# Kernel optimization log

Measured on AMD Instinct MI355X. Metric: run time of the kernel, lower is better.

Reference implementation:

```python
import jax, jax.numpy as jnp
import numpy as np

N = 50000   # nodes
D = 128     # hidden_dim == in_dim
H = 4       # heads
C = 32      # hidden_dim // heads
L = 3       # message_layers
ET = 640000 # temporal edges
EH = 320000 # host edges


def layer_norm(x, g, b, eps=1e-5):
    m = x.mean(-1, keepdims=True)
    v = ((x - m) ** 2).mean(-1, keepdims=True)
    return (x - m) / jnp.sqrt(v + eps) * g + b


def transformer_conv(h, src, dst, e_emb, Wq, bq, Wk, bk, Wv, bv, We, Ws, bs):
    # PyG TransformerConv, concat=True, root_weight=True, beta=False
    n = h.shape[0]
    q = (h @ Wq + bq).reshape(n, H, C)
    k = (h @ Wk + bk).reshape(n, H, C)
    v = (h @ Wv + bv).reshape(n, H, C)
    ee = (e_emb @ We).reshape(-1, H, C)          # lin_edge has no bias
    kj = k[src] + ee                              # [E,H,C]
    a = (q[dst] * kj).sum(-1) / np.sqrt(C)        # [E,H]
    amax = jax.ops.segment_max(a, dst, num_segments=n)
    amax = jnp.where(jnp.isfinite(amax), amax, 0.0)
    ex = jnp.exp(a - amax[dst])
    den = jax.ops.segment_sum(ex, dst, num_segments=n)
    alpha = ex / (den[dst] + 1e-16)               # segment softmax over in-edges of dst
    msg = (v[src] + ee) * alpha[..., None]        # [E,H,C]
    out = jax.ops.segment_sum(msg, dst, num_segments=n).reshape(n, H * C)
    return out + h @ Ws + bs                      # root/skip connection


def mlp_head(h, W1, b1, g, bt, W2, b2):
    z = jax.nn.silu(h @ W1 + b1)
    z = layer_norm(z, g, bt)
    return z @ W2 + b2


def setup_inputs() -> dict:
    key = jax.random.key(0)
    ks = iter(jax.random.split(key, 80))
    nrm = lambda shape: jax.random.normal(next(ks), shape, jnp.float32) * 0.05
    inp = {}
    inp['x'] = jax.random.normal(next(ks), (N, D), jnp.float32)
    inp['edge_index_temporal'] = jax.random.randint(next(ks), (2, ET), 0, N)
    inp['edge_index_host'] = jax.random.randint(next(ks), (2, EH), 0, N)
    inp['edge_attr_temporal'] = jax.random.uniform(next(ks), (ET, 1), jnp.float32)
    inp['edge_attr_host'] = jax.random.normal(next(ks), (EH, 3), jnp.float32)
    # edge encoders
    inp['W_tedge'] = nrm((1, 4)); inp['b_tedge'] = jnp.zeros(4)
    inp['W_hedge'] = nrm((3, 4)); inp['b_hedge'] = jnp.zeros(4)
    # stacked conv params [L, ...] for temporal (_t) and host (_h) convs
    for s in ('t', 'h'):
        inp[f'Wq_{s}'] = nrm((L, D, D)); inp[f'bq_{s}'] = jnp.zeros((L, D))
        inp[f'Wk_{s}'] = nrm((L, D, D)); inp[f'bk_{s}'] = jnp.zeros((L, D))
        inp[f'Wv_{s}'] = nrm((L, D, D)); inp[f'bv_{s}'] = jnp.zeros((L, D))
        inp[f'We_{s}'] = nrm((L, 4, D))
        inp[f'Ws_{s}'] = nrm((L, D, D)); inp[f'bs_{s}'] = jnp.zeros((L, D))
    inp['norm_g'] = jnp.ones((L, D)); inp['norm_b'] = jnp.zeros((L, D))
    inp['fg'] = jnp.ones(D); inp['fb'] = jnp.zeros(D)
    inp['dW1'] = nrm((D, D)); inp['db1'] = jnp.zeros(D)
    inp['dg'] = jnp.ones(D); inp['dbt'] = jnp.zeros(D)
    inp['dW2'] = nrm((D, 3)); inp['db2'] = jnp.zeros(3)
    inp['sW1'] = nrm((D, D)); inp['sb1'] = jnp.zeros(D)
    inp['sg'] = jnp.ones(D); inp['sbt'] = jnp.zeros(D)
    inp['sW2'] = nrm((D, 3)); inp['sb2'] = jnp.zeros(3)
    return inp


def reference(x, edge_index_temporal, edge_index_host, edge_attr_temporal, edge_attr_host,
              W_tedge, b_tedge, W_hedge, b_hedge,
              Wq_t, bq_t, Wk_t, bk_t, Wv_t, bv_t, We_t, Ws_t, bs_t,
              Wq_h, bq_h, Wk_h, bk_h, Wv_h, bv_h, We_h, Ws_h, bs_h,
              norm_g, norm_b, fg, fb,
              dW1, db1, dg, dbt, dW2, db2,
              sW1, sb1, sg, sbt, sW2, sb2):
    te = edge_attr_temporal @ W_tedge + b_tedge   # [ET, edge_dim]
    he = edge_attr_host @ W_hedge + b_hedge       # [EH, edge_dim]
    st, dt_ = edge_index_temporal[0], edge_index_temporal[1]
    sh, dh = edge_index_host[0], edge_index_host[1]
    h = x
    for l in range(L):
        t_out = transformer_conv(h, st, dt_, te, Wq_t[l], bq_t[l], Wk_t[l], bk_t[l],
                                 Wv_t[l], bv_t[l], We_t[l], Ws_t[l], bs_t[l])
        h_out = transformer_conv(h, sh, dh, he, Wq_h[l], bq_h[l], Wk_h[l], bk_h[l],
                                 Wv_h[l], bv_h[l], We_h[l], Ws_h[l], bs_h[l])
        combined = jax.nn.silu(layer_norm(t_out + h_out, norm_g[l], norm_b[l]))
        h = h + combined  # residual (shapes match since in_dim == hidden_dim)
    h = layer_norm(h, fg, fb)
    drift = mlp_head(h, dW1, db1, dg, dbt, dW2, db2)
    diff = mlp_head(h, sW1, sb1, sg, sbt, sW2, sb2)
    return drift, diff
```

## Files before the change

kernel.cpp:

```cpp
#include <hip/hip_runtime.h>
#include <math.h>

#define NN 50000
#define DD 128
#define ET_N 640000
#define EH_N 320000
#define NL 3

static inline int cdiv(int a, int b){ return (a+b-1)/b; }

typedef __attribute__((ext_vector_type(8))) short short8;
typedef __attribute__((ext_vector_type(4))) float f32x4;

__device__ float   g_h [(size_t)NN*DD];
__device__ unsigned short g_hb[(size_t)NN*DD];
__device__ unsigned short g_Wb[(size_t)NL*8*DD*DD];
__device__ float   g_Q [2][(size_t)NN*DD];
__device__ float   g_S [2][(size_t)NN*DD];
__device__ ushort2 g_KV[2][(size_t)NN*DD];
__device__ float   g_to[(size_t)NN*DD];
__device__ float   g_ho[(size_t)NN*DD];
__device__ int     g_cnt[2][NN];
__device__ int     g_cur[2][NN];
__device__ int     g_rs [2][NN+1];
__device__ int     g_srcc[2][ET_N];
__device__ float4  g_ee  [2][ET_N];

__device__ inline unsigned short f2bf(float f){
  unsigned u = __float_as_uint(f);
  unsigned r = (u + 0x7fffu + ((u>>16)&1u)) >> 16;
  return (unsigned short)r;
}
__device__ inline float bf2f(unsigned short s){
  return __uint_as_float(((unsigned)s)<<16);
}

__global__ void k_copy_h(const float* __restrict__ x){
  int i = blockIdx.x*256 + threadIdx.x;
  if (i < NN*DD/4){
    float4 v = reinterpret_cast<const float4*>(x)[i];
    reinterpret_cast<float4*>(g_h)[i] = v;
    ushort4 b; b.x=f2bf(v.x); b.y=f2bf(v.y); b.z=f2bf(v.z); b.w=f2bf(v.w);
    reinterpret_cast<ushort4*>(g_hb)[i] = b;
  }
}

__global__ void k_zero_cnt(){
  int i = blockIdx.x*256 + threadIdx.x;
  if (i < NN) g_cnt[blockIdx.y][i] = 0;
}

struct WPtrs { const float* W[24]; };
__global__ __launch_bounds__(256) void k_cvtw(WPtrs wp){
  int mat = blockIdx.y;
  const float* W = wp.W[mat];
  int e = blockIdx.x*256 + threadIdx.x;
  int n = e >> 7, k = e & 127;
  g_Wb[(size_t)mat*DD*DD + e] = f2bf(W[k*DD+n]);
}

__global__ void k_hist(const int* __restrict__ dstT, const int* __restrict__ dstH){
  int which = blockIdx.y;
  int E = which ? EH_N : ET_N;
  const int* dst = which ? dstH : dstT;
  int e = blockIdx.x*256+threadIdx.x;
  if (e<E) atomicAdd(&g_cnt[which][dst[e]], 1);
}

__global__ __launch_bounds__(1024) void k_scan(){
  int which = blockIdx.y;
  int* row_start = g_rs[which];
  const int* cnt = g_cnt[which];
  int* cur = g_cur[which];
  __shared__ int buf[1024];
  int tid = threadIdx.x;
  const int n = NN;
  int chunk = (n + 1023) >> 10;
  int start = tid*chunk; if (start>n) start=n;
  int end = start+chunk; if (end>n) end=n;
  int lsum=0;
  for (int i=start;i<end;++i) lsum += cnt[i];
  buf[tid]=lsum;
  __syncthreads();
  for (int off=1; off<1024; off<<=1){
    int t = (tid>=off)? buf[tid-off]:0;
    __syncthreads();
    buf[tid] += t;
    __syncthreads();
  }
  int run = buf[tid]-lsum;
  for (int i=start;i<end;++i){ row_start[i]=run; cur[i]=run; run += cnt[i]; }
  if (tid==1023) row_start[n]=run;
}

__global__ void k_scatter(const int* __restrict__ eit, const int* __restrict__ eih,
                          const float* __restrict__ attrT, const float* __restrict__ attrH,
                          const float* __restrict__ Wt, const float* __restrict__ bt4,
                          const float* __restrict__ Wh, const float* __restrict__ bh4){
  int which = blockIdx.y;
  int e = blockIdx.x*256+threadIdx.x;
  if (which==0){
    if (e>=ET_N) return;
    int src = eit[e], dst = eit[ET_N+e];
    int p = atomicAdd(&g_cur[0][dst],1);
    g_srcc[0][p]=src;
    float a = attrT[e];
    g_ee[0][p] = make_float4(a*Wt[0]+bt4[0], a*Wt[1]+bt4[1], a*Wt[2]+bt4[2], a*Wt[3]+bt4[3]);
  } else {
    if (e>=EH_N) return;
    int src = eih[e], dst = eih[EH_N+e];
    int p = atomicAdd(&g_cur[1][dst],1);
    g_srcc[1][p]=src;
    float a0=attrH[e*3+0], a1=attrH[e*3+1], a2=attrH[e*3+2];
    float4 v;
    v.x = a0*Wh[0]+a1*Wh[4]+a2*Wh[8]+bh4[0];
    v.y = a0*Wh[1]+a1*Wh[5]+a2*Wh[9]+bh4[1];
    v.z = a0*Wh[2]+a1*Wh[6]+a2*Wh[10]+bh4[2];
    v.w = a0*Wh[3]+a1*Wh[7]+a2*Wh[11]+bh4[3];
    g_ee[1][p] = v;
  }
}

struct BiasP { const float* b[8]; };

__global__ __launch_bounds__(256) void k_gemm_mfma(int l, BiasP bp){
  __shared__ unsigned short lA[64*DD];
  __shared__ unsigned short lB[DD*DD];
  int y = blockIdx.y;
  int conv = y/3, kind = y%3;
  int setbase = l*8 + conv*4;
  const unsigned short* Wm0 = &g_Wb[(size_t)(setbase + (kind==0?0:(kind==1?1:3)))*DD*DD];
  const unsigned short* Wm1 = &g_Wb[(size_t)(setbase+2)*DD*DD];
  int tid = threadIdx.x;
  int m0 = blockIdx.x*64;

#pragma unroll
  for (int p=0;p<4;++p){
    int c = tid + p*256;
    int row = c >> 4, col16 = c & 15;
    int grow = m0 + row;
    uint4 v = make_uint4(0,0,0,0);
    if (grow < NN) v = *reinterpret_cast<const uint4*>(&g_hb[(size_t)grow*DD + col16*8]);
    int off = (row*256 + col16*16) ^ ((row&7)<<4);
    *reinterpret_cast<uint4*>((char*)lA + off) = v;
  }
#pragma unroll
  for (int p=0;p<8;++p){
    int c = tid + p*256;
    int row = c >> 4, col16 = c & 15;
    uint4 v = *reinterpret_cast<const uint4*>(&Wm0[(size_t)row*DD + col16*8]);
    int off = (row*256 + col16*16) ^ ((row&7)<<4);
    *reinterpret_cast<uint4*>((char*)lB + off) = v;
  }
  __syncthreads();

  int wave = tid >> 6, lane = tid & 63;
  int lrow = lane & 15, kg = lane >> 4;
  int n0w = wave*32;

  short8 a[4][4];
#pragma unroll
  for (int kk=0;kk<4;++kk){
    int kbyte = kk*64 + kg*16;
#pragma unroll
    for (int mi=0;mi<4;++mi){
      int row = mi*16 + lrow;
      int off = (row*256 + kbyte) ^ ((row&7)<<4);
      a[kk][mi] = *reinterpret_cast<const short8*>((char*)lA + off);
    }
  }

  f32x4 acc[4][2];
#pragma unroll
  for (int mi=0;mi<4;++mi)
#pragma unroll
    for (int ni=0;ni<2;++ni) acc[mi][ni] = (f32x4){0.f,0.f,0.f,0.f};

#pragma unroll
  for (int kk=0;kk<4;++kk){
    int kbyte = kk*64 + kg*16;
    short8 b[2];
#pragma unroll
    for (int ni=0;ni<2;++ni){
      int n = n0w + ni*16 + lrow;
      int off = (n*256 + kbyte) ^ ((n&7)<<4);
      b[ni] = *reinterpret_cast<const short8*>((char*)lB + off);
    }
#pragma unroll
    for (int mi=0;mi<4;++mi)
#pragma unroll
      for (int ni=0;ni<2;++ni)
        acc[mi][ni] = __builtin_amdgcn_mfma_f32_16x16x32_bf16(a[kk][mi], b[ni], acc[mi][ni], 0,0,0);
  }

  f32x4 acc2[4][2];
  if (kind==1){
    __syncthreads();
#pragma unroll
    for (int p=0;p<8;++p){
      int c = tid + p*256;
      int row = c >> 4, col16 = c & 15;
      uint4 v = *reinterpret_cast<const uint4*>(&Wm1[(size_t)row*DD + col16*8]);
      int off = (row*256 + col16*16) ^ ((row&7)<<4);
      *reinterpret_cast<uint4*>((char*)lB + off) = v;
    }
    __syncthreads();
#pragma unroll
    for (int mi=0;mi<4;++mi)
#pragma unroll
      for (int ni=0;ni<2;++ni) acc2[mi][ni] = (f32x4){0.f,0.f,0.f,0.f};
#pragma unroll
    for (int kk=0;kk<4;++kk){
      int kbyte = kk*64 + kg*16;
      short8 b[2];
#pragma unroll
      for (int ni=0;ni<2;++ni){
        int n = n0w + ni*16 + lrow;
        int off = (n*256 + kbyte) ^ ((n&7)<<4);
        b[ni] = *reinterpret_cast<const short8*>((char*)lB + off);
      }
#pragma unroll
      for (int mi=0;mi<4;++mi)
#pragma unroll
        for (int ni=0;ni<2;++ni)
          acc2[mi][ni] = __builtin_amdgcn_mfma_f32_16x16x32_bf16(a[kk][mi], b[ni], acc2[mi][ni], 0,0,0);
    }
  }

  const float* bias0 = bp.b[conv*4 + (kind==0?0:(kind==1?1:3))];
  const float* bias1 = bp.b[conv*4 + 2];
#pragma unroll
  for (int ni=0;ni<2;++ni){
    int col = n0w + ni*16 + lrow;
    float bs0 = bias0[col];
    float bs1 = (kind==1) ? bias1[col] : 0.f;
#pragma unroll
    for (int mi=0;mi<4;++mi){
#pragma unroll
      for (int r=0;r<4;++r){
        int row = m0 + mi*16 + kg*4 + r;
        if (row >= NN) continue;
        size_t o = (size_t)row*DD + col;
        if (kind==1){
          ushort2 kv;
          kv.x = f2bf(acc[mi][ni][r]  + bs0);
          kv.y = f2bf(acc2[mi][ni][r] + bs1);
          g_KV[conv][o] = kv;
        } else {
          float* op = (kind==0) ? g_Q[conv] : g_S[conv];
          op[o] = acc[mi][ni][r] + bs0;
        }
      }
    }
  }
}

__global__ __launch_bounds__(128) void k_agg(const float* __restrict__ WeT,
                                             const float* __restrict__ WeH){
  int conv = blockIdx.y;
  int i = blockIdx.x;
  int d = threadIdx.x;
  const float* We = conv ? WeH : WeT;
  float w0=We[d], w1=We[DD+d], w2=We[2*DD+d], w3=We[3*DD+d];
  float qd = g_Q[conv][(size_t)i*DD+d];
  const int*     srcc = g_srcc[conv];
  const float4*  ee   = g_ee[conv];
  const ushort2* KV   = g_KV[conv];
  int beg=g_rs[conv][i], end=g_rs[conv][i+1];
  float m=-INFINITY, den=0.f, acc=0.f;
  if (beg<end){
    int s = srcc[beg];
    float4 e4 = ee[beg];
    ushort2 kv = KV[(size_t)s*DD+d];
    for (int idx=beg; idx<end; ++idx){
      ushort2 kv_n = kv; float4 e4_n = e4;
      if (idx+1<end){
        int s_n = srcc[idx+1];
        e4_n = ee[idx+1];
        kv_n = KV[(size_t)s_n*DD+d];
      }
      float eev = e4.x*w0 + e4.y*w1 + e4.z*w2 + e4.w*w3;
      float kf = bf2f(kv.x), vf = bf2f(kv.y);
      float p = qd*(kf+eev);
      p += __shfl_xor(p,16); p += __shfl_xor(p,8); p += __shfl_xor(p,4);
      p += __shfl_xor(p,2);  p += __shfl_xor(p,1);
      float a = p*0.17677669529663687f;
      float nm = fmaxf(m,a);
      float sc = __expf(m-nm);
      float ea = __expf(a-nm);
      den = den*sc + ea;
      acc = acc*sc + ea*(vf+eev);
      m = nm;
      kv = kv_n; e4 = e4_n;
    }
  }
  float r = acc/(den+1e-16f) + g_S[conv][(size_t)i*DD+d];
  float* o = conv ? g_ho : g_to;
  o[(size_t)i*DD+d] = r;
}

__device__ inline float waveRed(float v){
  v += __shfl_xor(v,32); v += __shfl_xor(v,16); v += __shfl_xor(v,8);
  v += __shfl_xor(v,4);  v += __shfl_xor(v,2);  v += __shfl_xor(v,1);
  return v;
}

__global__ __launch_bounds__(256) void k_combine(const float* __restrict__ g, const float* __restrict__ bt){
  int lane = threadIdx.x & 63;
  int node = blockIdx.x*4 + (threadIdx.x>>6);
  if (node>=NN) return;
  size_t i0 = (size_t)node*DD + lane, i1 = i0+64;
  float v0 = g_to[i0] + g_ho[i0];
  float v1 = g_to[i1] + g_ho[i1];
  float s = waveRed(v0+v1);
  float mean = s*(1.f/128.f);
  float d0=v0-mean, d1=v1-mean;
  float q = waveRed(d0*d0+d1*d1);
  float inv = 1.f/sqrtf(q*(1.f/128.f)+1e-5f);
  float c0 = d0*inv*g[lane]+bt[lane];
  float c1 = d1*inv*g[lane+64]+bt[lane+64];
  float h0 = g_h[i0] + c0/(1.f+expf(-c0));
  float h1 = g_h[i1] + c1/(1.f+expf(-c1));
  g_h[i0] = h0; g_h[i1] = h1;
  g_hb[i0] = f2bf(h0); g_hb[i1] = f2bf(h1);
}

__global__ __launch_bounds__(256) void k_finalln(const float* __restrict__ g, const float* __restrict__ b){
  int lane = threadIdx.x & 63;
  int node = blockIdx.x*4 + (threadIdx.x>>6);
  if (node>=NN) return;
  size_t i0 = (size_t)node*DD + lane, i1 = i0+64;
  float v0 = g_h[i0], v1 = g_h[i1];
  float s = waveRed(v0+v1);
  float mean = s*(1.f/128.f);
  float d0=v0-mean, d1=v1-mean;
  float q = waveRed(d0*d0+d1*d1);
  float inv = 1.f/sqrtf(q*(1.f/128.f)+1e-5f);
  g_h[i0]=d0*inv*g[lane]+b[lane];
  g_h[i1]=d1*inv*g[lane+64]+b[lane+64];
}

__global__ __launch_bounds__(128) void k_head(
      const float* __restrict__ W1, const float* __restrict__ b1,
      const float* __restrict__ g, const float* __restrict__ bt,
      const float* __restrict__ W2, const float* __restrict__ b2,
      float* __restrict__ out){
  int d = threadIdx.x;
  int wv = d >> 6;
  int i0 = blockIdx.x*8;
  const int n = NN;
  __shared__ float rows[8][DD];
  __shared__ float comb[2];
#pragma unroll
  for (int t=0;t<8;++t){
    int node = i0+t;
    rows[t][d] = (node<n)? g_h[(size_t)node*DD+d] : 0.f;
  }
  __syncthreads();
  float z[8];
  float b1d = b1[d];
#pragma unroll
  for (int t=0;t<8;++t) z[t]=b1d;
  for (int k=0;k<DD;++k){
    float w = W1[k*DD+d];
#pragma unroll
    for (int t=0;t<8;++t) z[t] += rows[t][k]*w;
  }
#pragma unroll
  for (int t=0;t<8;++t){ float v=z[t]; z[t] = v/(1.f+expf(-v)); }
  float gd=g[d], btd=bt[d];
  float w2a=W2[d*3+0], w2b=W2[d*3+1], w2c=W2[d*3+2];
  float b2a=b2[0], b2b=b2[1], b2c=b2[2];
  for (int t=0;t<8;++t){
    int node=i0+t;
    float zz=z[t];
    float s = waveRed(zz);
    if ((d&63)==0) comb[wv]=s;
    __syncthreads();
    float mean=(comb[0]+comb[1])*(1.f/128.f);
    __syncthreads();
    float dv=zz-mean;
    float q2 = waveRed(dv*dv);
    if ((d&63)==0) comb[wv]=q2;
    __syncthreads();
    float inv = 1.f/sqrtf((comb[0]+comb[1])*(1.f/128.f)+1e-5f);
    __syncthreads();
    float zn = dv*inv*gd+btd;
    float p0 = waveRed(zn*w2a);
    if ((d&63)==0) comb[wv]=p0;
    __syncthreads();
    float o0 = comb[0]+comb[1]+b2a;
    __syncthreads();
    float p1 = waveRed(zn*w2b);
    if ((d&63)==0) comb[wv]=p1;
    __syncthreads();
    float o1 = comb[0]+comb[1]+b2b;
    __syncthreads();
    float p2 = waveRed(zn*w2c);
    if ((d&63)==0) comb[wv]=p2;
    __syncthreads();
    float o2 = comb[0]+comb[1]+b2c;
    __syncthreads();
    if (d==0 && node<n){
      out[(size_t)node*3+0]=o0; out[(size_t)node*3+1]=o1; out[(size_t)node*3+2]=o2;
    }
  }
}

extern "C" void kernel_launch(void* const* d_in, const int* in_sizes, int n_in,
                              void* d_out, int out_size, void* d_ws, size_t ws_size,
                              hipStream_t stream){
  (void)in_sizes; (void)n_in; (void)out_size; (void)d_ws; (void)ws_size;
  const float* x    = (const float*)d_in[0];
  const int*   eit  = (const int*)d_in[1];
  const int*   eih  = (const int*)d_in[2];
  const float* eat  = (const float*)d_in[3];
  const float* eah  = (const float*)d_in[4];
  const float* W_te = (const float*)d_in[5];
  const float* b_te = (const float*)d_in[6];
  const float* W_he = (const float*)d_in[7];
  const float* b_he = (const float*)d_in[8];
  const float *Wq_t=(const float*)d_in[9],  *bq_t=(const float*)d_in[10];
  const float *Wk_t=(const float*)d_in[11], *bk_t=(const float*)d_in[12];
  const float *Wv_t=(const float*)d_in[13], *bv_t=(const float*)d_in[14];
  const float *We_t=(const float*)d_in[15];
  const float *Ws_t=(const float*)d_in[16], *bs_t=(const float*)d_in[17];
  const float *Wq_h=(const float*)d_in[18], *bq_h=(const float*)d_in[19];
  const float *Wk_h=(const float*)d_in[20], *bk_h=(const float*)d_in[21];
  const float *Wv_h=(const float*)d_in[22], *bv_h=(const float*)d_in[23];
  const float *We_h=(const float*)d_in[24];
  const float *Ws_h=(const float*)d_in[25], *bs_h=(const float*)d_in[26];
  const float *norm_g=(const float*)d_in[27], *norm_b=(const float*)d_in[28];
  const float *fg=(const float*)d_in[29], *fb=(const float*)d_in[30];
  const float *dW1=(const float*)d_in[31], *db1=(const float*)d_in[32];
  const float *dg=(const float*)d_in[33],  *dbt=(const float*)d_in[34];
  const float *dW2=(const float*)d_in[35], *db2=(const float*)d_in[36];
  const float *sW1=(const float*)d_in[37], *sb1=(const float*)d_in[38];
  const float *sg=(const float*)d_in[39],  *sbt=(const float*)d_in[40];
  const float *sW2=(const float*)d_in[41], *sb2=(const float*)d_in[42];
  float* outp = (float*)d_out;

  k_copy_h<<<cdiv(NN*DD/4,256),256,0,stream>>>(x);

  WPtrs wp;
  for (int l=0;l<NL;++l){
    wp.W[l*8+0]=Wq_t+(size_t)l*DD*DD; wp.W[l*8+1]=Wk_t+(size_t)l*DD*DD;
    wp.W[l*8+2]=Wv_t+(size_t)l*DD*DD; wp.W[l*8+3]=Ws_t+(size_t)l*DD*DD;
    wp.W[l*8+4]=Wq_h+(size_t)l*DD*DD; wp.W[l*8+5]=Wk_h+(size_t)l*DD*DD;
    wp.W[l*8+6]=Wv_h+(size_t)l*DD*DD; wp.W[l*8+7]=Ws_h+(size_t)l*DD*DD;
  }
  k_cvtw<<<dim3(64,24),256,0,stream>>>(wp);

  k_zero_cnt<<<dim3(cdiv(NN,256),2),256,0,stream>>>();
  k_hist<<<dim3(cdiv(ET_N,256),2),256,0,stream>>>(eit+ET_N, eih+EH_N);
  k_scan<<<dim3(1,2),1024,0,stream>>>();
  k_scatter<<<dim3(cdiv(ET_N,256),2),256,0,stream>>>(eit, eih, eat, eah, W_te, b_te, W_he, b_he);

  for (int l=0;l<NL;++l){
    BiasP bp;
    bp.b[0]=bq_t+(size_t)l*DD; bp.b[1]=bk_t+(size_t)l*DD;
    bp.b[2]=bv_t+(size_t)l*DD; bp.b[3]=bs_t+(size_t)l*DD;
    bp.b[4]=bq_h+(size_t)l*DD; bp.b[5]=bk_h+(size_t)l*DD;
    bp.b[6]=bv_h+(size_t)l*DD; bp.b[7]=bs_h+(size_t)l*DD;
    k_gemm_mfma<<<dim3(cdiv(NN,64),6),256,0,stream>>>(l, bp);
    k_agg<<<dim3(NN,2),128,0,stream>>>(We_t+(size_t)l*4*DD, We_h+(size_t)l*4*DD);
    k_combine<<<cdiv(NN,4),256,0,stream>>>(norm_g+(size_t)l*DD, norm_b+(size_t)l*DD);
  }
  k_finalln<<<cdiv(NN,4),256,0,stream>>>(fg, fb);
  k_head<<<cdiv(NN,8),128,0,stream>>>(dW1, db1, dg, dbt, dW2, db2, outp);
  k_head<<<cdiv(NN,8),128,0,stream>>>(sW1, sb1, sg, sbt, sW2, sb2, outp+(size_t)NN*3);
}
```

Before: 1.384 ms.

## Fuse edge aggregation with layernorm combine and fold edge encoder into We

Merges the per-conv aggregation and the combine/layernorm/residual kernel into one block per node that handles both convs, exchanging through shared memory. This removes the g_to/g_ho intermediate round trips and one launch per layer. It also stores raw edge attributes (a float for temporal edges, a float4 for host edges) instead of 4-wide encoded embeddings, folding the edge encoder into per-dimension coefficients, which cuts the temporal edge stream traffic. The cost is that the two convs in a block now have unequal degree loops, so the faster half idles at the barrier.

```diff
diff --git a/kernel.cpp b/kernel.cpp
--- a/kernel.cpp
+++ b/kernel.cpp
@@ -18,13 +18,12 @@
 __device__ float   g_Q [2][(size_t)NN*DD];
 __device__ float   g_S [2][(size_t)NN*DD];
 __device__ ushort2 g_KV[2][(size_t)NN*DD];
-__device__ float   g_to[(size_t)NN*DD];
-__device__ float   g_ho[(size_t)NN*DD];
 __device__ int     g_cnt[2][NN];
 __device__ int     g_cur[2][NN];
 __device__ int     g_rs [2][NN+1];
 __device__ int     g_srcc[2][ET_N];
-__device__ float4  g_ee  [2][ET_N];
+__device__ float   g_ta[ET_N];
+__device__ float4  g_ha[EH_N];
 
 __device__ inline unsigned short f2bf(float f){
   unsigned u = __float_as_uint(f);
@@ -94,9 +93,7 @@
 }
 
 __global__ void k_scatter(const int* __restrict__ eit, const int* __restrict__ eih,
-                          const float* __restrict__ attrT, const float* __restrict__ attrH,
-                          const float* __restrict__ Wt, const float* __restrict__ bt4,
-                          const float* __restrict__ Wh, const float* __restrict__ bh4){
+                          const float* __restrict__ attrT, const float* __restrict__ attrH){
   int which = blockIdx.y;
   int e = blockIdx.x*256+threadIdx.x;
   if (which==0){
@@ -104,20 +101,13 @@
     int src = eit[e], dst = eit[ET_N+e];
     int p = atomicAdd(&g_cur[0][dst],1);
     g_srcc[0][p]=src;
-    float a = attrT[e];
-    g_ee[0][p] = make_float4(a*Wt[0]+bt4[0], a*Wt[1]+bt4[1], a*Wt[2]+bt4[2], a*Wt[3]+bt4[3]);
+    g_ta[p]=attrT[e];
   } else {
     if (e>=EH_N) return;
     int src = eih[e], dst = eih[EH_N+e];
     int p = atomicAdd(&g_cur[1][dst],1);
     g_srcc[1][p]=src;
-    float a0=attrH[e*3+0], a1=attrH[e*3+1], a2=attrH[e*3+2];
-    float4 v;
-    v.x = a0*Wh[0]+a1*Wh[4]+a2*Wh[8]+bh4[0];
-    v.y = a0*Wh[1]+a1*Wh[5]+a2*Wh[9]+bh4[1];
-    v.z = a0*Wh[2]+a1*Wh[6]+a2*Wh[10]+bh4[2];
-    v.w = a0*Wh[3]+a1*Wh[7]+a2*Wh[11]+bh4[3];
-    g_ee[1][p] = v;
+    g_ha[p]=make_float4(attrH[e*3+0],attrH[e*3+1],attrH[e*3+2],0.f);
   }
 }
 
@@ -255,31 +245,53 @@
   }
 }
 
-__global__ __launch_bounds__(128) void k_agg(const float* __restrict__ WeT,
-                                             const float* __restrict__ WeH){
-  int conv = blockIdx.y;
+__device__ inline float waveRed(float v){
+  v += __shfl_xor(v,32); v += __shfl_xor(v,16); v += __shfl_xor(v,8);
+  v += __shfl_xor(v,4);  v += __shfl_xor(v,2);  v += __shfl_xor(v,1);
+  return v;
+}
+
+__global__ __launch_bounds__(256) void k_aggc(
+    const float* __restrict__ WeT, const float* __restrict__ WeH,
+    const float* __restrict__ Wt,  const float* __restrict__ bt4,
+    const float* __restrict__ Wh,  const float* __restrict__ bh4,
+    const float* __restrict__ ng,  const float* __restrict__ nb){
+  int tid = threadIdx.x;
+  int conv = tid >> 7;
+  int d = tid & 127;
   int i = blockIdx.x;
-  int d = threadIdx.x;
-  const float* We = conv ? WeH : WeT;
-  float w0=We[d], w1=We[DD+d], w2=We[2*DD+d], w3=We[3*DD+d];
+
+  float c0=0.f,c1=0.f,c2=0.f,c3=0.f;
+  if (conv==0){
+#pragma unroll
+    for (int j=0;j<4;++j){ float w=WeT[j*DD+d]; c1 += Wt[j]*w; c0 += bt4[j]*w; }
+  } else {
+#pragma unroll
+    for (int j=0;j<4;++j){
+      float w=WeH[j*DD+d];
+      c0 += Wh[j]*w; c1 += Wh[4+j]*w; c2 += Wh[8+j]*w; c3 += bh4[j]*w;
+    }
+  }
+
   float qd = g_Q[conv][(size_t)i*DD+d];
   const int*     srcc = g_srcc[conv];
-  const float4*  ee   = g_ee[conv];
   const ushort2* KV   = g_KV[conv];
   int beg=g_rs[conv][i], end=g_rs[conv][i+1];
   float m=-INFINITY, den=0.f, acc=0.f;
   if (beg<end){
     int s = srcc[beg];
-    float4 e4 = ee[beg];
+    float4 at = make_float4(0.f,0.f,0.f,0.f);
+    if (conv==0) at.x = g_ta[beg]; else at = g_ha[beg];
     ushort2 kv = KV[(size_t)s*DD+d];
     for (int idx=beg; idx<end; ++idx){
-      ushort2 kv_n = kv; float4 e4_n = e4;
+      ushort2 kv_n = kv; float4 at_n = at;
       if (idx+1<end){
         int s_n = srcc[idx+1];
-        e4_n = ee[idx+1];
+        if (conv==0) at_n.x = g_ta[idx+1]; else at_n = g_ha[idx+1];
         kv_n = KV[(size_t)s_n*DD+d];
       }
-      float eev = e4.x*w0 + e4.y*w1 + e4.z*w2 + e4.w*w3;
+      float eev = (conv==0) ? fmaf(at.x, c1, c0)
+                            : (at.x*c0 + at.y*c1 + at.z*c2 + c3);
       float kf = bf2f(kv.x), vf = bf2f(kv.y);
       float p = qd*(kf+eev);
       p += __shfl_xor(p,16); p += __shfl_xor(p,8); p += __shfl_xor(p,4);
@@ -291,38 +303,32 @@
       den = den*sc + ea;
       acc = acc*sc + ea*(vf+eev);
       m = nm;
-      kv = kv_n; e4 = e4_n;
+      kv = kv_n; at = at_n;
     }
   }
   float r = acc/(den+1e-16f) + g_S[conv][(size_t)i*DD+d];
-  float* o = conv ? g_ho : g_to;
-  o[(size_t)i*DD+d] = r;
-}
-
-__device__ inline float waveRed(float v){
-  v += __shfl_xor(v,32); v += __shfl_xor(v,16); v += __shfl_xor(v,8);
-  v += __shfl_xor(v,4);  v += __shfl_xor(v,2);  v += __shfl_xor(v,1);
-  return v;
-}
-
-__global__ __launch_bounds__(256) void k_combine(const float* __restrict__ g, const float* __restrict__ bt){
-  int lane = threadIdx.x & 63;
-  int node = blockIdx.x*4 + (threadIdx.x>>6);
-  if (node>=NN) return;
-  size_t i0 = (size_t)node*DD + lane, i1 = i0+64;
-  float v0 = g_to[i0] + g_ho[i0];
-  float v1 = g_to[i1] + g_ho[i1];
-  float s = waveRed(v0+v1);
-  float mean = s*(1.f/128.f);
-  float d0=v0-mean, d1=v1-mean;
-  float q = waveRed(d0*d0+d1*d1);
-  float inv = 1.f/sqrtf(q*(1.f/128.f)+1e-5f);
-  float c0 = d0*inv*g[lane]+bt[lane];
-  float c1 = d1*inv*g[lane+64]+bt[lane+64];
-  float h0 = g_h[i0] + c0/(1.f+expf(-c0));
-  float h1 = g_h[i1] + c1/(1.f+expf(-c1));
-  g_h[i0] = h0; g_h[i1] = h1;
-  g_hb[i0] = f2bf(h0); g_hb[i1] = f2bf(h1);
+
+  __shared__ float xch[DD];
+  __shared__ float red[4];
+  if (conv==1) xch[d] = r;
+  __syncthreads();
+  float v = (conv==0) ? (r + xch[d]) : 0.f;
+  float s1 = waveRed(v);
+  if ((tid&63)==0) red[tid>>6] = s1;
+  __syncthreads();
+  float mean = (red[0]+red[1])*(1.f/128.f);
+  float dv = v - mean;
+  float q2 = waveRed(dv*dv);
+  __syncthreads();
+  if ((tid&63)==0) red[tid>>6] = q2;
+  __syncthreads();
+  if (conv==0){
+    float inv = 1.f/sqrtf((red[0]+red[1])*(1.f/128.f)+1e-5f);
+    float c = dv*inv*ng[d] + nb[d];
+    size_t o = (size_t)i*DD+d;
+    float h = g_h[o] + c/(1.f+__expf(-c));
+    g_h[o]=h; g_hb[o]=f2bf(h);
+  }
 }
 
 __global__ __launch_bounds__(256) void k_finalln(const float* __restrict__ g, const float* __restrict__ b){
@@ -454,7 +460,7 @@
   k_zero_cnt<<<dim3(cdiv(NN,256),2),256,0,stream>>>();
   k_hist<<<dim3(cdiv(ET_N,256),2),256,0,stream>>>(eit+ET_N, eih+EH_N);
   k_scan<<<dim3(1,2),1024,0,stream>>>();
-  k_scatter<<<dim3(cdiv(ET_N,256),2),256,0,stream>>>(eit, eih, eat, eah, W_te, b_te, W_he, b_he);
+  k_scatter<<<dim3(cdiv(ET_N,256),2),256,0,stream>>>(eit, eih, eat, eah);
 
   for (int l=0;l<NL;++l){
     BiasP bp;
@@ -463,8 +469,9 @@
     bp.b[4]=bq_h+(size_t)l*DD; bp.b[5]=bk_h+(size_t)l*DD;
     bp.b[6]=bv_h+(size_t)l*DD; bp.b[7]=bs_h+(size_t)l*DD;
     k_gemm_mfma<<<dim3(cdiv(NN,64),6),256,0,stream>>>(l, bp);
-    k_agg<<<dim3(NN,2),128,0,stream>>>(We_t+(size_t)l*4*DD, We_h+(size_t)l*4*DD);
-    k_combine<<<cdiv(NN,4),256,0,stream>>>(norm_g+(size_t)l*DD, norm_b+(size_t)l*DD);
+    k_aggc<<<NN,256,0,stream>>>(We_t+(size_t)l*4*DD, We_h+(size_t)l*4*DD,
+                                W_te, b_te, W_he, b_he,
+                                norm_g+(size_t)l*DD, norm_b+(size_t)l*DD);
   }
   k_finalln<<<cdiv(NN,4),256,0,stream>>>(fg, fb);
   k_head<<<cdiv(NN,8),128,0,stream>>>(dW1, db1, dg, dbt, dW2, db2, outp);
```

After: 1.662 ms. 20.1% more time.
